# Kernel optimization log

Hardware: AMD Instinct MI355X
Metric: run time of the kernel (lower is better)

## Reference

```python
import jax, jax.numpy as jnp
import numpy as np
import math

B, N, L, ED, H = 2, 32, 4, 64, 4   # graphs, nodes/graph, layers, embed_dim, heads
HD = ED // H
EPS = 1e-5


def _ln(x, g, b):
    m = x.mean(-1, keepdims=True)
    v = ((x - m) ** 2).mean(-1, keepdims=True)
    return (x - m) * jax.lax.rsqrt(v + EPS) * g + b


def _layer(x, W, b, lg, lb, fW, fb, fg, fbeta):
    # NOTE: in the torch source, ModuleList([Linear]*4) shares ONE linear for
    # q/k/v1/v2 and ONE LayerNorm for norms[0..2]; we reproduce that sharing.
    h = (x @ W.T + b).reshape(B, N, N, H, HD)
    q = _ln(h, lg, lb)                                    # q == k (shared LN)
    scores = jnp.einsum('bxahd,bayhd->bxayh', q, q) / math.sqrt(HD)
    att = jax.nn.softmax(scores, axis=2)                  # softmax over 'a'
    xu = jnp.einsum('bxahd,bayhd->bxayhd', h, h)          # v1 == v2 == h
    xu = _ln(xu, lg, lb)                                  # shared LN again
    xu = jnp.einsum('bxayh,bxayhd->bxyhd', att, xu).reshape(B, N, N, ED)
    y = jnp.concatenate([x, xu], axis=-1) @ fW.T + fb
    return _ln(y, fg, fbeta)


def _diag_offdiag_maxpool(x):
    # x: (B, ED, N, N)
    diag = jnp.diagonal(x, axis1=-2, axis2=-1)            # (B, ED, N)
    max_diag = diag.max(axis=2)                           # (B, ED)
    val = jnp.abs(max_diag.max() + (-x).max())
    eye = jnp.eye(N, dtype=x.dtype)
    max_offdiag = (x - val * eye).max(axis=(2, 3))        # (B, ED)
    return jnp.concatenate([max_diag, max_offdiag], axis=1)  # (B, 2*ED)


def setup_inputs() -> dict:
    key = jax.random.key(0)
    ks = jax.random.split(key, 12)
    E = 1024
    g = jax.random.randint(ks[0], (E,), 0, B)
    ls = jax.random.randint(ks[1], (E,), 0, N)
    ld = jax.random.randint(ks[2], (E,), 0, N)
    edge_index = jnp.stack([g * N + ls, g * N + ld]).astype(jnp.int64)
    batch = (jnp.arange(B * N) // N).astype(jnp.int64)
    std = 0.02
    return {
        'edge_index': edge_index,
        'batch': batch,
        'W0': jax.random.normal(ks[3], (ED, 1), jnp.float32) * std,
        'b0': jnp.zeros((ED,), jnp.float32),
        'Ws': jax.random.normal(ks[4], (L - 1, ED, ED), jnp.float32) * std,
        'bs': jnp.zeros((L - 1, ED), jnp.float32),
        'ln_g': jnp.ones((L, HD), jnp.float32),
        'ln_b': jnp.zeros((L, HD), jnp.float32),
        'fW0': jax.random.normal(ks[5], (ED, 1 + ED), jnp.float32) * std,
        'fb0': jnp.zeros((ED,), jnp.float32),
        'fWs': jax.random.normal(ks[6], (L - 1, ED, 2 * ED), jnp.float32) * std,
        'fbs': jnp.zeros((L - 1, ED), jnp.float32),
        'fln_g': jnp.ones((L, ED), jnp.float32),
        'fln_b': jnp.zeros((L, ED), jnp.float32),
        'opW': jax.random.normal(ks[7], (L, ED // 2, 2 * ED), jnp.float32) * std,
        'opb': jnp.zeros((L, ED // 2), jnp.float32),
    }


def reference(edge_index, batch, W0, b0, Ws, bs, ln_g, ln_b,
              fW0, fb0, fWs, fbs, fln_g, fln_b, opW, opb):
    # to_dense_adj with edge_attr = 1.0
    g = batch[edge_index[0]]
    ls = edge_index[0] - g * N
    ld = edge_index[1] - g * N
    adj = jnp.zeros((B, N, N), jnp.float32).at[g, ls, ld].add(1.0)
    idx = jnp.arange(N)
    adj = adj.at[:, idx, idx].set(2.0)
    x = adj[..., None]                                    # (B, N, N, 1)

    scores = jnp.zeros((B, ED // 2), jnp.float32)
    for i in range(L):
        W = W0 if i == 0 else Ws[i - 1]
        b = b0 if i == 0 else bs[i - 1]
        fW = fW0 if i == 0 else fWs[i - 1]
        fb = fb0 if i == 0 else fbs[i - 1]
        x = _layer(x, W, b, ln_g[i], ln_b[i], fW, fb, fln_g[i], fln_b[i])
        pooled = _diag_offdiag_maxpool(jnp.transpose(x, (0, 3, 1, 2)))
        scores = scores + pooled @ opW[i].T + opb[i]

    # BatchNorm1d(momentum=1.0, affine=False), training mode -> batch stats
    m = scores.mean(axis=0)
    v = scores.var(axis=0)
    return (scores - m) / jnp.sqrt(v + EPS)
```

## Files before the change

kernel.cpp:

```cpp
#include <hip/hip_runtime.h>
#include <math.h>

#define EPS 1e-5f

#define AG_LOAD(p)     __hip_atomic_load((p), __ATOMIC_RELAXED, __HIP_MEMORY_SCOPE_AGENT)

__device__ __forceinline__ unsigned fenc(float f) {
    unsigned u = __float_as_uint(f);
    return (u & 0x80000000u) ? ~u : (u | 0x80000000u);
}
__device__ __forceinline__ float fdec(unsigned u) {
    u = (u & 0x80000000u) ? (u & 0x7FFFFFFFu) : ~u;
    return __uint_as_float(u);
}

struct Params {
    const int* ei; const int* batch; int E;
    const float* W0; const float* b0; const float* Ws; const float* bs;
    const float* ln_g; const float* ln_b;
    const float* fW0; const float* fb0; const float* fWs; const float* fbs;
    const float* fln_g; const float* fln_b;
    const float* opW; const float* opb;
    float* hA; float* hAT;
    float* hB; float* hBT;
    float* xbuf;
    unsigned* PdgU; unsigned* PoffU; unsigned* PmnU;
    int* bar;
    float* out;
};


__device__ __forceinline__ void pool_atomic(Params& p, int layer, int b_blk, int e,
                                            float mn, float off, float dg) {
    int o = layer * 128 + b_blk * 64 + e;
    atomicMax(&p.PdgU[o],  fenc(dg));
    atomicMax(&p.PoffU[o], fenc(off));
    atomicMax(&p.PmnU[o],  fenc(-mn));
}

__launch_bounds__(256, 2)
__global__ void k0(Params p) {
    const int tid  = threadIdx.x;
    const int blk  = blockIdx.x;
    const int gtid = blk * 256 + tid;
    const int c    = tid & 63;
    const int d    = c & 15;
    const int rl   = tid >> 6;
    const int rx   = rl >> 1;
    const int ry   = rl & 1;
    const int b_blk = blk >> 8;
    const int x0    = ((blk >> 4) & 15) * 2;
    const int y0    = (blk & 15) * 2;
    const int a_l  = c & 31;
    const int h1   = c >> 5;

    __shared__ float xslab2[2 * 32];
    __shared__ float yslab2[32 * 2];
    __shared__ __align__(16) float cA[64], cC[64], cW[64], cB0[64], cG[64], cBl[64];
    __shared__ float hstat[3][4];
    __shared__ float A1_s[4 * 132];
    __shared__ float K0h_s[4][4];
    __shared__ __align__(16) float xrow[4][64];
    __shared__ __align__(16) float xu_s[4][64];
    __shared__ float Wf0[64];
    __shared__ __align__(16) float T65[64 * 68];
    __shared__ __align__(16) float ST[64 * 68];

    if (tid < 64)  xslab2[tid] = 0.0f;
    if (tid >= 64 && tid < 128) yslab2[tid - 64] = 0.0f;

    if (tid < 64) {
        float Wc = p.W0[c], bc = p.b0[c];
        float sW = Wc, sB = bc;
        #pragma unroll
        for (int m = 1; m < 16; m <<= 1) {
            sW += __shfl_xor(sW, m, 16);
            sB += __shfl_xor(sB, m, 16);
        }
        float Ac = Wc - sW * 0.0625f;
        float Bc = bc - sB * 0.0625f;
        float sAA = Ac * Ac, sAB = Ac * Bc, sBB = Bc * Bc;
        #pragma unroll
        for (int m = 1; m < 16; m <<= 1) {
            sAA += __shfl_xor(sAA, m, 16);
            sAB += __shfl_xor(sAB, m, 16);
            sBB += __shfl_xor(sBB, m, 16);
        }
        cA[c] = Ac; cC[c] = Bc; cW[c] = Wc; cB0[c] = bc;
        cG[c] = p.ln_g[d]; cBl[c] = p.ln_b[d];
        if (d == 0) {
            hstat[0][c >> 4] = sAA * 0.0625f;
            hstat[1][c >> 4] = sAB * 0.0625f;
            hstat[2][c >> 4] = sBB * 0.0625f;
        }
        Wf0[tid] = p.fW0[tid * 65];
    }
    #pragma unroll
    for (int s = 0; s < 4; ++s) {
        int i = tid + s * 256;
        int cc = i >> 4, u = i & 15;
        const float* src = p.fW0 + cc * 65 + 1 + 4 * u;
        float4 w = make_float4(src[0], src[1], src[2], src[3]);
        *(float4*)(T65 + cc * 68 + 4 * ((u + 2 * cc) & 15)) = w;
    }
    #pragma unroll
    for (int s = 0; s < 4; ++s) {
        int i = tid + s * 256;
        float4 w = ((const float4*)p.Ws)[i];
        int cc = i >> 4, u = i & 15;
        *(float4*)(ST + cc * 68 + 4 * ((u + 2 * cc) & 15)) = w;
    }
    __syncthreads();

    for (int e2 = tid; e2 < p.E; e2 += 256) {
        int e0 = p.ei[e2], e1 = p.ei[p.E + e2];
        int g  = p.batch[e0];
        if (g == b_blk) {
            int ls = e0 - g * 32, ld = e1 - g * 32;
            unsigned dx = (unsigned)(ls - x0);
            if (dx < 2u) atomicAdd(&xslab2[dx * 32 + ld], 1.0f);
            unsigned dy = (unsigned)(ld - y0);
            if (dy < 2u) atomicAdd(&yslab2[ls * 2 + dy], 1.0f);
        }
    }
    __syncthreads();
    if (tid < 2)  xslab2[tid * 32 + x0 + tid] = 2.0f;
    if (tid >= 2 && tid < 4) { int j = tid - 2; yslab2[(y0 + j) * 2 + j] = 2.0f; }
    __syncthreads();

    const float vx = xslab2[rx * 32 + a_l];
    const float vy = yslab2[a_l * 2 + ry];
    float s0, s1, is0, is1, w0m, w1m;
    #pragma unroll
    for (int hb = 0; hb < 2; ++hb) {
        const int hh = h1 + 2 * hb;
        float rsx = rsqrtf(fmaf(fmaf(hstat[0][hh], vx, 2.0f * hstat[1][hh]), vx, hstat[2][hh]) + EPS);
        float rsy = rsqrtf(fmaf(fmaf(hstat[0][hh], vy, 2.0f * hstat[1][hh]), vy, hstat[2][hh]) + EPS);
        float qq = 0.f, sp = 0.f, sq = 0.f;
        #pragma unroll
        for (int t = 0; t < 4; ++t) {
            int dd = hh * 16 + 4 * t;
            float4 av = *(const float4*)(cA + dd);
            float4 bv = *(const float4*)(cC + dd);
            float4 wv = *(const float4*)(cW + dd);
            float4 b0v = *(const float4*)(cB0 + dd);
            float4 gv = *(const float4*)(cG + dd);
            float4 blv = *(const float4*)(cBl + dd);
            float qx, qy, pp;
            qx = fmaf(av.x, vx, bv.x) * rsx * gv.x + blv.x;
            qy = fmaf(av.x, vy, bv.x) * rsy * gv.x + blv.x;
            qq = fmaf(qx, qy, qq);
            pp = fmaf(wv.x, vx, b0v.x) * fmaf(wv.x, vy, b0v.x); sp += pp; sq += pp * pp;
            qx = fmaf(av.y, vx, bv.y) * rsx * gv.y + blv.y;
            qy = fmaf(av.y, vy, bv.y) * rsy * gv.y + blv.y;
            qq = fmaf(qx, qy, qq);
            pp = fmaf(wv.y, vx, b0v.y) * fmaf(wv.y, vy, b0v.y); sp += pp; sq += pp * pp;
            qx = fmaf(av.z, vx, bv.z) * rsx * gv.z + blv.z;
            qy = fmaf(av.z, vy, bv.z) * rsy * gv.z + blv.z;
            qq = fmaf(qx, qy, qq);
            pp = fmaf(wv.z, vx, b0v.z) * fmaf(wv.z, vy, b0v.z); sp += pp; sq += pp * pp;
            qx = fmaf(av.w, vx, bv.w) * rsx * gv.w + blv.w;
            qy = fmaf(av.w, vy, bv.w) * rsy * gv.w + blv.w;
            qq = fmaf(qx, qy, qq);
            pp = fmaf(wv.w, vx, b0v.w) * fmaf(wv.w, vy, b0v.w); sp += pp; sq += pp * pp;
        }
        float ss = qq * 0.25f;
        float mu = sp * 0.0625f, var = fmaxf(sq * 0.0625f - mu * mu, 0.f);
        float is = rsqrtf(var + EPS);
        if (hb == 0) { s0 = ss; is0 = is; w0m = mu * is; }
        else         { s1 = ss; is1 = is; w1m = mu * is; }
    }

    float m0 = s0, m1 = s1;
    #pragma unroll
    for (int m = 1; m < 32; m <<= 1) {
        m0 = fmaxf(m0, __shfl_xor(m0, m));
        m1 = fmaxf(m1, __shfl_xor(m1, m));
    }
    float e0 = __expf(s0 - m0), e1 = __expf(s1 - m1);
    float l0 = e0, l1 = e1, k0a = e0 * w0m, k1a = e1 * w1m;
    #pragma unroll
    for (int m = 1; m < 32; m <<= 1) {
        l0 += __shfl_xor(l0, m);  l1 += __shfl_xor(l1, m);
        k0a += __shfl_xor(k0a, m); k1a += __shfl_xor(k1a, m);
    }
    A1_s[rl * 132 + h1 * 33 + a_l]       = e0 * is0 / l0;
    A1_s[rl * 132 + (h1 + 2) * 33 + a_l] = e1 * is1 / l1;
    if (a_l == 0) {
        K0h_s[rl][h1]     = k0a / l0;
        K0h_s[rl][h1 + 2] = k1a / l1;
    }

    {
        const int hc = c >> 4;
        const float Wc = cW[c], bc = cB0[c];
        float acc = 0.f;
        #pragma unroll
        for (int a = 0; a < 32; ++a) {
            float vx2 = xslab2[rx * 32 + a];
            float vy2 = yslab2[a * 2 + ry];
            float pv = fmaf(Wc, vx2, bc) * fmaf(Wc, vy2, bc);
            acc = fmaf(A1_s[rl * 132 + hc * 33 + a], pv, acc);
        }
        xu_s[rl][c] = (acc - K0h_s[rl][hc]) * cG[c] + cBl[c];
    }

    const float adjv = xslab2[rx * 32 + y0 + ry];
    float acc2 = fmaf(Wf0[c], adjv, p.fb0[c]);
    #pragma unroll
    for (int u = 0; u < 16; ++u) {
        float4 w = *(const float4*)(T65 + c * 68 + 4 * ((u + 2 * c) & 15));
        float4 xr = *(const float4*)(&xu_s[rl][4 * u]);
        acc2 = fmaf(w.x, xr.x, acc2); acc2 = fmaf(w.y, xr.y, acc2);
        acc2 = fmaf(w.z, xr.z, acc2); acc2 = fmaf(w.w, xr.w, acc2);
    }
    float t1 = acc2;
    #pragma unroll
    for (int m = 1; m < 64; m <<= 1) t1 += __shfl_xor(t1, m, 64);
    float mu = t1 * (1.0f / 64.0f);
    float dv2 = acc2 - mu;
    float t2 = dv2 * dv2;
    #pragma unroll
    for (int m = 1; m < 64; m <<= 1) t2 += __shfl_xor(t2, m, 64);
    float xnew = dv2 * rsqrtf(t2 * (1.0f / 64.0f) + EPS) * p.fln_g[c] + p.fln_b[c];
    xrow[rl][c]  = xnew;
    p.xbuf[gtid] = xnew;
    __syncthreads();

    if (tid < 64) {
        float mn = 1e30f, off = -1e30f, dg = -1e30f;
        #pragma unroll
        for (int r2 = 0; r2 < 4; ++r2) {
            float v = xrow[r2][tid];
            mn = fminf(mn, v);
            if (x0 + (r2 >> 1) == y0 + (r2 & 1)) dg = fmaxf(dg, v);
            else off = fmaxf(off, v);
        }
        pool_atomic(p, 0, b_blk, tid, mn, off, dg);
    }

    {
        float acc = p.bs[c];
        #pragma unroll
        for (int u = 0; u < 16; ++u) {
            float4 w = *(const float4*)(ST + c * 68 + 4 * ((u + 2 * c) & 15));
            float4 xr = *(const float4*)(&xrow[rl][4 * u]);
            acc = fmaf(w.x, xr.x, acc); acc = fmaf(w.y, xr.y, acc);
            acc = fmaf(w.z, xr.z, acc); acc = fmaf(w.w, xr.w, acc);
        }
        int x = x0 + rx, y = y0 + ry;
        p.hA[(b_blk * 1024 + x * 32 + y) * 64 + c] = acc;
        p.hAT[((b_blk * 32 + y) * 32 + x) * 64 + c] = acc;
    }
}

__launch_bounds__(256, 2)
__global__ void klayer(Params p, int layer, int is_last) {
    const int tid  = threadIdx.x;
    const int blk  = blockIdx.x;
    const int gtid = blk * 256 + tid;
    const int c    = tid & 63;
    const int d    = c & 15;
    const int rl   = tid >> 6;
    const int rx   = rl >> 1;
    const int ry   = rl & 1;
    const int b_blk = blk >> 8;
    const int x0    = ((blk >> 4) & 15) * 2;
    const int y0    = (blk & 15) * 2;
    const int a_l  = c & 31;
    const int h1   = c >> 5;

    const float* hin  = (layer == 2) ? p.hB  : p.hA;
    const float* hinT = (layer == 2) ? p.hBT : p.hAT;
    float* hout  = (layer == 1) ? p.hB  : p.hA;
    float* houtT = (layer == 1) ? p.hBT : p.hAT;

    __shared__ __align__(16) float hx2_s[2][2176];
    __shared__ __align__(16) float yT2_s[2][2176];
    __shared__ __align__(16) float FT[64 * 132];
    __shared__ float A1_s[4 * 132];
    __shared__ float K0h_s[4][4];
    __shared__ __align__(16) float xrow[4][64];
    __shared__ __align__(16) float xu_s[4][64];
    __shared__ __align__(16) float g16[16], b16[16];
    __shared__ float vals[4];
    __shared__ float scores_s[64];
    __shared__ int tailflag;
    float* sm_mn  = &hx2_s[0][0];
    float* sm_off = sm_mn + 512;
    float* sm_dg  = sm_mn + 1024;
    float* psum   = sm_mn + 1536;

    float xv = p.xbuf[gtid];
    {
        const float4* sx0 = (const float4*)(hin + (b_blk * 1024 + x0 * 32) * 64);
        const float4* sx1 = (const float4*)(hin + (b_blk * 1024 + (x0 + 1) * 32) * 64);
        const float4* sy0 = (const float4*)(hinT + (b_blk * 32 + y0) * 2048);
        const float4* sy1 = (const float4*)(hinT + (b_blk * 32 + y0 + 1) * 2048);
        #pragma unroll
        for (int s = 0; s < 2; ++s) {
            int ii = tid + s * 256;
            int a = ii >> 4, u = ii & 15, pr = (u + 2 * a) & 15;
            *(float4*)(&hx2_s[0][a * 68 + 4 * pr]) = sx0[ii];
            *(float4*)(&hx2_s[1][a * 68 + 4 * pr]) = sx1[ii];
            *(float4*)(&yT2_s[0][a * 68 + 4 * pr]) = sy0[ii];
            *(float4*)(&yT2_s[1][a * 68 + 4 * pr]) = sy1[ii];
        }
    }
    if (tid < 16) {
        g16[tid] = p.ln_g[layer * 16 + tid];
        b16[tid] = p.ln_b[layer * 16 + tid];
    }
    {
        const float4* fw = (const float4*)(p.fWs + (layer - 1) * 8192);
        #pragma unroll
        for (int s = 0; s < 8; ++s) {
            int i = tid + s * 256;
            float4 w = fw[i];
            int cc = i >> 5, u = i & 31;
            *(float4*)(FT + cc * 132 + 4 * ((u + 2 * cc) & 31)) = w;
        }
    }
    xrow[rl][c] = xv;
    __syncthreads();

    float s0, s1, is0, is1, w0m, w1m;
    #pragma unroll
    for (int hb = 0; hb < 2; ++hb) {
        const int hh = h1 + 2 * hb;
        float4 xh4[4], yh4[4];
        float sxp = 0.f, sxq = 0.f, syp = 0.f, syq = 0.f;
        #pragma unroll
        for (int t = 0; t < 4; ++t) {
            int ps = 4 * (((hh * 4 + t) + 2 * a_l) & 15);
            float4 v = *(const float4*)(&hx2_s[rx][a_l * 68 + ps]);
            float4 y = *(const float4*)(&yT2_s[ry][a_l * 68 + ps]);
            xh4[t] = v; yh4[t] = y;
            sxp += v.x + v.y + v.z + v.w;
            sxq += v.x*v.x + v.y*v.y + v.z*v.z + v.w*v.w;
            syp += y.x + y.y + y.z + y.w;
            syq += y.x*y.x + y.y*y.y + y.z*y.z + y.w*y.w;
        }
        float mxm = sxp * 0.0625f;
        float rsx = rsqrtf(fmaxf(sxq * 0.0625f - mxm * mxm, 0.f) + EPS);
        float mym = syp * 0.0625f;
        float rsy = rsqrtf(fmaxf(syq * 0.0625f - mym * mym, 0.f) + EPS);
        float qq = 0.f, sp = 0.f, sq = 0.f;
        #pragma unroll
        for (int t = 0; t < 4; ++t) {
            float4 g4 = *(const float4*)(g16 + 4 * t);
            float4 b4 = *(const float4*)(b16 + 4 * t);
            float4 xh = xh4[t], yh = yh4[t];
            float qx, qy, pp;
            qx = (xh.x - mxm) * rsx * g4.x + b4.x;
            qy = (yh.x - mym) * rsy * g4.x + b4.x;
            qq = fmaf(qx, qy, qq);  pp = xh.x * yh.x; sp += pp; sq += pp * pp;
            qx = (xh.y - mxm) * rsx * g4.y + b4.y;
            qy = (yh.y - mym) * rsy * g4.y + b4.y;
            qq = fmaf(qx, qy, qq);  pp = xh.y * yh.y; sp += pp; sq += pp * pp;
            qx = (xh.z - mxm) * rsx * g4.z + b4.z;
            qy = (yh.z - mym) * rsy * g4.z + b4.z;
            qq = fmaf(qx, qy, qq);  pp = xh.z * yh.z; sp += pp; sq += pp * pp;
            qx = (xh.w - mxm) * rsx * g4.w + b4.w;
            qy = (yh.w - mym) * rsy * g4.w + b4.w;
            qq = fmaf(qx, qy, qq);  pp = xh.w * yh.w; sp += pp; sq += pp * pp;
        }
        float ss = qq * 0.25f;
        float mu = sp * 0.0625f, var = fmaxf(sq * 0.0625f - mu * mu, 0.f);
        float is = rsqrtf(var + EPS);
        if (hb == 0) { s0 = ss; is0 = is; w0m = mu * is; }
        else         { s1 = ss; is1 = is; w1m = mu * is; }
    }

    float m0 = s0, m1 = s1;
    #pragma unroll
    for (int m = 1; m < 32; m <<= 1) {
        m0 = fmaxf(m0, __shfl_xor(m0, m));
        m1 = fmaxf(m1, __shfl_xor(m1, m));
    }
    float e0 = __expf(s0 - m0), e1 = __expf(s1 - m1);
    float l0 = e0, l1 = e1, k0a = e0 * w0m, k1a = e1 * w1m;
    #pragma unroll
    for (int m = 1; m < 32; m <<= 1) {
        l0 += __shfl_xor(l0, m);  l1 += __shfl_xor(l1, m);
        k0a += __shfl_xor(k0a, m); k1a += __shfl_xor(k1a, m);
    }
    A1_s[rl * 132 + h1 * 33 + a_l]       = e0 * is0 / l0;
    A1_s[rl * 132 + (h1 + 2) * 33 + a_l] = e1 * is1 / l1;
    if (a_l == 0) {
        K0h_s[rl][h1]     = k0a / l0;
        K0h_s[rl][h1 + 2] = k1a / l1;
    }

    {
        const int hc = c >> 4;
        const int ce = c & 3;
        float acc = 0.f;
        #pragma unroll
        for (int a = 0; a < 32; ++a) {
            int ps = 4 * (((c >> 2) + 2 * a) & 15) + ce;
            float hxv = hx2_s[rx][a * 68 + ps];
            float hyv = yT2_s[ry][a * 68 + ps];
            acc = fmaf(A1_s[rl * 132 + hc * 33 + a], hxv * hyv, acc);
        }
        xu_s[rl][c] = (acc - K0h_s[rl][hc]) * g16[d] + b16[d];
    }

    float acc2 = p.fbs[(layer - 1) * 64 + c];
    #pragma unroll
    for (int u = 0; u < 16; ++u) {
        float4 w = *(const float4*)(FT + c * 132 + 4 * ((u + 2 * c) & 31));
        float4 xr = *(const float4*)(&xrow[rl][4 * u]);
        acc2 = fmaf(w.x, xr.x, acc2); acc2 = fmaf(w.y, xr.y, acc2);
        acc2 = fmaf(w.z, xr.z, acc2); acc2 = fmaf(w.w, xr.w, acc2);
    }
    #pragma unroll
    for (int u = 16; u < 32; ++u) {
        float4 w = *(const float4*)(FT + c * 132 + 4 * ((u + 2 * c) & 31));
        float4 xr = *(const float4*)(&xu_s[rl][4 * (u - 16)]);
        acc2 = fmaf(w.x, xr.x, acc2); acc2 = fmaf(w.y, xr.y, acc2);
        acc2 = fmaf(w.z, xr.z, acc2); acc2 = fmaf(w.w, xr.w, acc2);
    }
    float t1 = acc2;
    #pragma unroll
    for (int m = 1; m < 64; m <<= 1) t1 += __shfl_xor(t1, m, 64);
    float mu = t1 * (1.0f / 64.0f);
    float dv2 = acc2 - mu;
    float t2 = dv2 * dv2;
    #pragma unroll
    for (int m = 1; m < 64; m <<= 1) t2 += __shfl_xor(t2, m, 64);
    float xnew = dv2 * rsqrtf(t2 * (1.0f / 64.0f) + EPS) *
                 p.fln_g[layer * 64 + c] + p.fln_b[layer * 64 + c];
    __syncthreads();
    xrow[rl][c] = xnew;
    if (!is_last) {
        p.xbuf[gtid] = xnew;
        const float4* sw = (const float4*)(p.Ws + layer * 4096);
        #pragma unroll
        for (int s = 0; s < 4; ++s) {
            int i = tid + s * 256;
            float4 w = sw[i];
            int cc = i >> 4, u = i & 15;
            *(float4*)(FT + cc * 68 + 4 * ((u + 2 * cc) & 15)) = w;
        }
    }
    __syncthreads();

    if (tid < 64) {
        float mn = 1e30f, off = -1e30f, dg = -1e30f;
        #pragma unroll
        for (int r2 = 0; r2 < 4; ++r2) {
            float v = xrow[r2][tid];
            mn = fminf(mn, v);
            if (x0 + (r2 >> 1) == y0 + (r2 & 1)) dg = fmaxf(dg, v);
            else off = fmaxf(off, v);
        }
        pool_atomic(p, layer, b_blk, tid, mn, off, dg);
    }

    if (!is_last) {
        float acc = p.bs[layer * 64 + c];
        #pragma unroll
        for (int u = 0; u < 16; ++u) {
            float4 w = *(const float4*)(FT + c * 68 + 4 * ((u + 2 * c) & 15));
            float4 xr = *(const float4*)(&xrow[rl][4 * u]);
            acc = fmaf(w.x, xr.x, acc); acc = fmaf(w.y, xr.y, acc);
            acc = fmaf(w.z, xr.z, acc); acc = fmaf(w.w, xr.w, acc);
        }
        int x = x0 + rx, y = y0 + ry;
        hout[(b_blk * 1024 + x * 32 + y) * 64 + c] = acc;
        houtT[((b_blk * 32 + y) * 32 + x) * 64 + c] = acc;
        return;
    }

    __syncthreads();
    if (tid == 0) {
        int r = __hip_atomic_fetch_add(p.bar, 1, __ATOMIC_RELAXED,
                                       __HIP_MEMORY_SCOPE_AGENT);
        tailflag = (r == 511) ? 1 : 0;
    }
    __syncthreads();
    if (!tailflag) return;

    #pragma unroll
    for (int s = 0; s < 2; ++s) {
        int slot = tid + s * 256;
        unsigned ud = AG_LOAD(&p.PdgU[slot]);
        unsigned uo = AG_LOAD(&p.PoffU[slot]);
        unsigned um = AG_LOAD(&p.PmnU[slot]);
        sm_dg[slot]  = fdec(ud);
        sm_off[slot] = fdec(uo);
        sm_mn[slot]  = -fdec(um);
    }
    __syncthreads();
    if (tid < 4) {
        float gmx = -1e30f, gmn = 1e30f;
        for (int i2 = 0; i2 < 128; ++i2) {
            gmx = fmaxf(gmx, sm_dg[tid * 128 + i2]);
            gmn = fminf(gmn, sm_mn[tid * 128 + i2]);
        }
        vals[tid] = fabsf(gmx - gmn);
    }
    __syncthreads();
    {
        int bb = tid >> 7, cc = (tid >> 2) & 31, pp = tid & 3;
        float a2 = 0.0f;
        for (int l = 0; l < 4; ++l) {
            float val = vals[l];
            const float* Wr = p.opW + l * 4096 + cc * 128;
            int base = l * 128 + bb * 64;
            for (int j = pp * 32; j < pp * 32 + 32; ++j) {
                float pv;
                if (j < 64) pv = sm_dg[base + j];
                else        pv = fmaxf(sm_off[base + j - 64], sm_dg[base + j - 64] - val);
                a2 = fmaf(Wr[j], pv, a2);
            }
        }
        psum[tid] = a2;
    }
    __syncthreads();
    if (tid < 64) {
        int bb = tid >> 5, cc = tid & 31;
        float a2 = 0.0f;
        for (int l = 0; l < 4; ++l) a2 += p.opb[l * 32 + cc];
        for (int pp = 0; pp < 4; ++pp) a2 += psum[bb * 128 + cc * 4 + pp];
        scores_s[tid] = a2;
    }
    __syncthreads();
    if (tid < 32) {
        float sA = scores_s[tid], sB = scores_s[32 + tid];
        float mu2 = 0.5f * (sA + sB);
        float va = 0.5f * ((sA - mu2) * (sA - mu2) + (sB - mu2) * (sB - mu2));
        float inv = rsqrtf(va + EPS);
        p.out[tid]      = (sA - mu2) * inv;
        p.out[32 + tid] = (sB - mu2) * inv;
    }
}

extern "C" void kernel_launch(void* const* d_in, const int* in_sizes, int n_in,
                              void* d_out, int out_size, void* d_ws, size_t ws_size,
                              hipStream_t stream) {
    Params prm;
    prm.ei    = (const int*)d_in[0];
    prm.batch = (const int*)d_in[1];
    prm.E     = in_sizes[0] / 2;
    prm.W0    = (const float*)d_in[2];
    prm.b0    = (const float*)d_in[3];
    prm.Ws    = (const float*)d_in[4];
    prm.bs    = (const float*)d_in[5];
    prm.ln_g  = (const float*)d_in[6];
    prm.ln_b  = (const float*)d_in[7];
    prm.fW0   = (const float*)d_in[8];
    prm.fb0   = (const float*)d_in[9];
    prm.fWs   = (const float*)d_in[10];
    prm.fbs   = (const float*)d_in[11];
    prm.fln_g = (const float*)d_in[12];
    prm.fln_b = (const float*)d_in[13];
    prm.opW   = (const float*)d_in[14];
    prm.opb   = (const float*)d_in[15];

    float* ws = (float*)d_ws;
    prm.hA    = ws;
    prm.hAT   = prm.hA   + 131072;
    prm.hB    = prm.hAT  + 131072;
    prm.hBT   = prm.hB   + 131072;
    prm.xbuf  = prm.hBT  + 131072;
    unsigned* pu = (unsigned*)(prm.xbuf + 131072);
    prm.PdgU  = pu;
    prm.PoffU = pu + 512;
    prm.PmnU  = pu + 1024;
    prm.bar   = (int*)(pu + 1536);
    prm.out   = (float*)d_out;

    hipMemsetAsync(pu, 0, 1552 * sizeof(unsigned), stream);
    k0<<<512, 256, 0, stream>>>(prm);
    klayer<<<512, 256, 0, stream>>>(prm, 1, 0);
    klayer<<<512, 256, 0, stream>>>(prm, 2, 0);
    klayer<<<512, 256, 0, stream>>>(prm, 3, 1);
}
```

Before: 160.7 us.

## Fuse layers 0 and 1 by recomputing layer-0 halo rows per block

Merges the first-layer kernel into the second layer. Each block rebuilds the full adjacency in shared memory and recomputes the layer-0 output for the 64 row and 64 column neighbours of its 2x2 tile (32 iterations per wave). It keeps the resulting layer-1 projections in shared slabs, so layer 1 runs without a launch boundary or a global round-trip. This removes one kernel launch and the hA/hAT traffic but adds heavy redundant compute and much larger shared memory, which may lower occupancy.

```diff
diff --git a/kernel.cpp b/kernel.cpp
--- a/kernel.cpp
+++ b/kernel.cpp
@@ -39,7 +39,7 @@
 }
 
 __launch_bounds__(256, 2)
-__global__ void k0(Params p) {
+__global__ void k1(Params p) {
     const int tid  = threadIdx.x;
     const int blk  = blockIdx.x;
     const int gtid = blk * 256 + tid;
@@ -54,21 +54,20 @@
     const int a_l  = c & 31;
     const int h1   = c >> 5;
 
-    __shared__ float xslab2[2 * 32];
-    __shared__ float yslab2[32 * 2];
+    __shared__ float adjm[32 * 33];
+    __shared__ __align__(16) float slabX[2][2176];
+    __shared__ __align__(16) float slabY[2][2176];
+    __shared__ __align__(16) float WB[8704];
     __shared__ __align__(16) float cA[64], cC[64], cW[64], cB0[64], cG[64], cBl[64];
     __shared__ float hstat[3][4];
+    __shared__ float Wf0[64];
     __shared__ float A1_s[4 * 132];
     __shared__ float K0h_s[4][4];
     __shared__ __align__(16) float xrow[4][64];
     __shared__ __align__(16) float xu_s[4][64];
-    __shared__ float Wf0[64];
-    __shared__ __align__(16) float T65[64 * 68];
-    __shared__ __align__(16) float ST[64 * 68];
-
-    if (tid < 64)  xslab2[tid] = 0.0f;
-    if (tid >= 64 && tid < 128) yslab2[tid - 64] = 0.0f;
-
+    __shared__ __align__(16) float g16[16], b16[16];
+
+    for (int i = tid; i < 1056; i += 256) adjm[i] = 0.0f;
     if (tid < 64) {
         float Wc = p.W0[c], bc = p.b0[c];
         float sW = Wc, sB = bc;
@@ -95,20 +94,24 @@
         }
         Wf0[tid] = p.fW0[tid * 65];
     }
+    if (tid < 16) {
+        g16[tid] = p.ln_g[16 + tid];
+        b16[tid] = p.ln_b[16 + tid];
+    }
     #pragma unroll
     for (int s = 0; s < 4; ++s) {
         int i = tid + s * 256;
         int cc = i >> 4, u = i & 15;
         const float* src = p.fW0 + cc * 65 + 1 + 4 * u;
         float4 w = make_float4(src[0], src[1], src[2], src[3]);
-        *(float4*)(T65 + cc * 68 + 4 * ((u + 2 * cc) & 15)) = w;
+        *(float4*)(WB + cc * 68 + 4 * ((u + 2 * cc) & 15)) = w;
     }
     #pragma unroll
     for (int s = 0; s < 4; ++s) {
         int i = tid + s * 256;
         float4 w = ((const float4*)p.Ws)[i];
         int cc = i >> 4, u = i & 15;
-        *(float4*)(ST + cc * 68 + 4 * ((u + 2 * cc) & 15)) = w;
+        *(float4*)(WB + 4352 + cc * 68 + 4 * ((u + 2 * cc) & 15)) = w;
     }
     __syncthreads();
 
@@ -117,52 +120,197 @@
         int g  = p.batch[e0];
         if (g == b_blk) {
             int ls = e0 - g * 32, ld = e1 - g * 32;
-            unsigned dx = (unsigned)(ls - x0);
-            if (dx < 2u) atomicAdd(&xslab2[dx * 32 + ld], 1.0f);
-            unsigned dy = (unsigned)(ld - y0);
-            if (dy < 2u) atomicAdd(&yslab2[ls * 2 + dy], 1.0f);
-        }
-    }
-    __syncthreads();
-    if (tid < 2)  xslab2[tid * 32 + x0 + tid] = 2.0f;
-    if (tid >= 2 && tid < 4) { int j = tid - 2; yslab2[(y0 + j) * 2 + j] = 2.0f; }
-    __syncthreads();
-
-    const float vx = xslab2[rx * 32 + a_l];
-    const float vy = yslab2[a_l * 2 + ry];
+            atomicAdd(&adjm[ls * 33 + ld], 1.0f);
+        }
+    }
+    __syncthreads();
+    if (tid < 32) adjm[tid * 33 + tid] = 2.0f;
+    __syncthreads();
+
+    #pragma unroll 1
+    for (int k = 0; k < 32; ++k) {
+        const int r = rl * 32 + k;
+        const bool isX = (r < 64);
+        const int rowx = isX ? (x0 + (r >> 5)) : ((r - 64) >> 1);
+        const int coly = isX ? (r & 31) : (y0 + ((r - 64) & 1));
+        const float vx = adjm[rowx * 33 + a_l];
+        const float vy = adjm[a_l * 33 + coly];
+
+        float s0, s1, is0, is1, w0m, w1m;
+        #pragma unroll
+        for (int hb = 0; hb < 2; ++hb) {
+            const int hh = h1 + 2 * hb;
+            float rsx = rsqrtf(fmaf(fmaf(hstat[0][hh], vx, 2.0f * hstat[1][hh]), vx, hstat[2][hh]) + EPS);
+            float rsy = rsqrtf(fmaf(fmaf(hstat[0][hh], vy, 2.0f * hstat[1][hh]), vy, hstat[2][hh]) + EPS);
+            float qq = 0.f, sp = 0.f, sq = 0.f;
+            #pragma unroll
+            for (int t = 0; t < 4; ++t) {
+                int dd = hh * 16 + 4 * t;
+                float4 av = *(const float4*)(cA + dd);
+                float4 bv = *(const float4*)(cC + dd);
+                float4 wv = *(const float4*)(cW + dd);
+                float4 b0v = *(const float4*)(cB0 + dd);
+                float4 gv = *(const float4*)(cG + dd);
+                float4 blv = *(const float4*)(cBl + dd);
+                float qx, qy, pp;
+                qx = fmaf(av.x, vx, bv.x) * rsx * gv.x + blv.x;
+                qy = fmaf(av.x, vy, bv.x) * rsy * gv.x + blv.x;
+                qq = fmaf(qx, qy, qq);
+                pp = fmaf(wv.x, vx, b0v.x) * fmaf(wv.x, vy, b0v.x); sp += pp; sq += pp * pp;
+                qx = fmaf(av.y, vx, bv.y) * rsx * gv.y + blv.y;
+                qy = fmaf(av.y, vy, bv.y) * rsy * gv.y + blv.y;
+                qq = fmaf(qx, qy, qq);
+                pp = fmaf(wv.y, vx, b0v.y) * fmaf(wv.y, vy, b0v.y); sp += pp; sq += pp * pp;
+                qx = fmaf(av.z, vx, bv.z) * rsx * gv.z + blv.z;
+                qy = fmaf(av.z, vy, bv.z) * rsy * gv.z + blv.z;
+                qq = fmaf(qx, qy, qq);
+                pp = fmaf(wv.z, vx, b0v.z) * fmaf(wv.z, vy, b0v.z); sp += pp; sq += pp * pp;
+                qx = fmaf(av.w, vx, bv.w) * rsx * gv.w + blv.w;
+                qy = fmaf(av.w, vy, bv.w) * rsy * gv.w + blv.w;
+                qq = fmaf(qx, qy, qq);
+                pp = fmaf(wv.w, vx, b0v.w) * fmaf(wv.w, vy, b0v.w); sp += pp; sq += pp * pp;
+            }
+            float ss = qq * 0.25f;
+            float mu = sp * 0.0625f, var = fmaxf(sq * 0.0625f - mu * mu, 0.f);
+            float is = rsqrtf(var + EPS);
+            if (hb == 0) { s0 = ss; is0 = is; w0m = mu * is; }
+            else         { s1 = ss; is1 = is; w1m = mu * is; }
+        }
+
+        float m0 = s0, m1 = s1;
+        #pragma unroll
+        for (int m = 1; m < 32; m <<= 1) {
+            m0 = fmaxf(m0, __shfl_xor(m0, m));
+            m1 = fmaxf(m1, __shfl_xor(m1, m));
+        }
+        float e0 = __expf(s0 - m0), e1 = __expf(s1 - m1);
+        float l0 = e0, l1 = e1, k0a = e0 * w0m, k1a = e1 * w1m;
+        #pragma unroll
+        for (int m = 1; m < 32; m <<= 1) {
+            l0 += __shfl_xor(l0, m);  l1 += __shfl_xor(l1, m);
+            k0a += __shfl_xor(k0a, m); k1a += __shfl_xor(k1a, m);
+        }
+        A1_s[rl * 132 + h1 * 33 + a_l]       = e0 * is0 / l0;
+        A1_s[rl * 132 + (h1 + 2) * 33 + a_l] = e1 * is1 / l1;
+        if (a_l == 0) {
+            K0h_s[rl][h1]     = k0a / l0;
+            K0h_s[rl][h1 + 2] = k1a / l1;
+        }
+
+        {
+            const int hc = c >> 4;
+            const float Wc = cW[c], bc = cB0[c];
+            float accp = 0.f;
+            #pragma unroll
+            for (int a = 0; a < 32; ++a) {
+                float vx2 = adjm[rowx * 33 + a];
+                float vy2 = adjm[a * 33 + coly];
+                float pv = fmaf(Wc, vx2, bc) * fmaf(Wc, vy2, bc);
+                accp = fmaf(A1_s[rl * 132 + hc * 33 + a], pv, accp);
+            }
+            xu_s[rl][c] = (accp - K0h_s[rl][hc]) * cG[c] + cBl[c];
+        }
+
+        const float adjv = adjm[rowx * 33 + coly];
+        float acc2 = fmaf(Wf0[c], adjv, p.fb0[c]);
+        #pragma unroll
+        for (int u = 0; u < 16; ++u) {
+            float4 w = *(const float4*)(WB + c * 68 + 4 * ((u + 2 * c) & 15));
+            float4 xr = *(const float4*)(&xu_s[rl][4 * u]);
+            acc2 = fmaf(w.x, xr.x, acc2); acc2 = fmaf(w.y, xr.y, acc2);
+            acc2 = fmaf(w.z, xr.z, acc2); acc2 = fmaf(w.w, xr.w, acc2);
+        }
+        float t1 = acc2;
+        #pragma unroll
+        for (int m = 1; m < 64; m <<= 1) t1 += __shfl_xor(t1, m, 64);
+        float mu = t1 * (1.0f / 64.0f);
+        float dv2 = acc2 - mu;
+        float t2 = dv2 * dv2;
+        #pragma unroll
+        for (int m = 1; m < 64; m <<= 1) t2 += __shfl_xor(t2, m, 64);
+        float x1c = dv2 * rsqrtf(t2 * (1.0f / 64.0f) + EPS) * p.fln_g[c] + p.fln_b[c];
+
+        if (isX && (unsigned)(coly - y0) < 2u)
+            xrow[(rowx - x0) * 2 + (coly - y0)][c] = x1c;
+        xu_s[rl][c] = x1c;
+
+        float acch = p.bs[c];
+        #pragma unroll
+        for (int u = 0; u < 16; ++u) {
+            float4 w = *(const float4*)(WB + 4352 + c * 68 + 4 * ((u + 2 * c) & 15));
+            float4 xr = *(const float4*)(&xu_s[rl][4 * u]);
+            acch = fmaf(w.x, xr.x, acch); acch = fmaf(w.y, xr.y, acch);
+            acch = fmaf(w.z, xr.z, acch); acch = fmaf(w.w, xr.w, acch);
+        }
+        float* srow = isX ? &slabX[r >> 5][0] : &slabY[(r - 64) & 1][0];
+        const int arow = isX ? (r & 31) : ((r - 64) >> 1);
+        srow[arow * 68 + 4 * (((c >> 2) + 2 * arow) & 15) + (c & 3)] = acch;
+    }
+    __syncthreads();
+
+    if (tid < 64) {
+        float mn = 1e30f, off = -1e30f, dg = -1e30f;
+        #pragma unroll
+        for (int r2 = 0; r2 < 4; ++r2) {
+            float v = xrow[r2][tid];
+            mn = fminf(mn, v);
+            if (x0 + (r2 >> 1) == y0 + (r2 & 1)) dg = fmaxf(dg, v);
+            else off = fmaxf(off, v);
+        }
+        pool_atomic(p, 0, b_blk, tid, mn, off, dg);
+    }
+    {
+        const float4* fw = (const float4*)(p.fWs);
+        #pragma unroll
+        for (int s = 0; s < 8; ++s) {
+            int i = tid + s * 256;
+            float4 w = fw[i];
+            int cc = i >> 5, u = i & 31;
+            *(float4*)(WB + cc * 132 + 4 * ((u + 2 * cc) & 31)) = w;
+        }
+    }
+    __syncthreads();
+
     float s0, s1, is0, is1, w0m, w1m;
     #pragma unroll
     for (int hb = 0; hb < 2; ++hb) {
         const int hh = h1 + 2 * hb;
-        float rsx = rsqrtf(fmaf(fmaf(hstat[0][hh], vx, 2.0f * hstat[1][hh]), vx, hstat[2][hh]) + EPS);
-        float rsy = rsqrtf(fmaf(fmaf(hstat[0][hh], vy, 2.0f * hstat[1][hh]), vy, hstat[2][hh]) + EPS);
+        float4 xh4[4], yh4[4];
+        float sxp = 0.f, sxq = 0.f, syp = 0.f, syq = 0.f;
+        #pragma unroll
+        for (int t = 0; t < 4; ++t) {
+            int ps = 4 * (((hh * 4 + t) + 2 * a_l) & 15);
+            float4 v = *(const float4*)(&slabX[rx][a_l * 68 + ps]);
+            float4 y = *(const float4*)(&slabY[ry][a_l * 68 + ps]);
+            xh4[t] = v; yh4[t] = y;
+            sxp += v.x + v.y + v.z + v.w;
+            sxq += v.x*v.x + v.y*v.y + v.z*v.z + v.w*v.w;
+            syp += y.x + y.y + y.z + y.w;
+            syq += y.x*y.x + y.y*y.y + y.z*y.z + y.w*y.w;
+        }
+        float mxm = sxp * 0.0625f;
+        float rsx = rsqrtf(fmaxf(sxq * 0.0625f - mxm * mxm, 0.f) + EPS);
+        float mym = syp * 0.0625f;
+        float rsy = rsqrtf(fmaxf(syq * 0.0625f - mym * mym, 0.f) + EPS);
         float qq = 0.f, sp = 0.f, sq = 0.f;
         #pragma unroll
         for (int t = 0; t < 4; ++t) {
-            int dd = hh * 16 + 4 * t;
-            float4 av = *(const float4*)(cA + dd);
-            float4 bv = *(const float4*)(cC + dd);
-            float4 wv = *(const float4*)(cW + dd);
-            float4 b0v = *(const float4*)(cB0 + dd);
-            float4 gv = *(const float4*)(cG + dd);
-            float4 blv = *(const float4*)(cBl + dd);
+            float4 g4 = *(const float4*)(g16 + 4 * t);
+            float4 b4 = *(const float4*)(b16 + 4 * t);
+            float4 xh = xh4[t], yh = yh4[t];
             float qx, qy, pp;
-            qx = fmaf(av.x, vx, bv.x) * rsx * gv.x + blv.x;
-            qy = fmaf(av.x, vy, bv.x) * rsy * gv.x + blv.x;
-            qq = fmaf(qx, qy, qq);
-            pp = fmaf(wv.x, vx, b0v.x) * fmaf(wv.x, vy, b0v.x); sp += pp; sq += pp * pp;
-            qx = fmaf(av.y, vx, bv.y) * rsx * gv.y + blv.y;
-            qy = fmaf(av.y, vy, bv.y) * rsy * gv.y + blv.y;
-            qq = fmaf(qx, qy, qq);
-            pp = fmaf(wv.y, vx, b0v.y) * fmaf(wv.y, vy, b0v.y); sp += pp; sq += pp * pp;
-            qx = fmaf(av.z, vx, bv.z) * rsx * gv.z + blv.z;
-            qy = fmaf(av.z, vy, bv.z) * rsy * gv.z + blv.z;
-            qq = fmaf(qx, qy, qq);
-            pp = fmaf(wv.z, vx, b0v.z) * fmaf(wv.z, vy, b0v.z); sp += pp; sq += pp * pp;
-            qx = fmaf(av.w, vx, bv.w) * rsx * gv.w + blv.w;
-            qy = fmaf(av.w, vy, bv.w) * rsy * gv.w + blv.w;
-            qq = fmaf(qx, qy, qq);
-            pp = fmaf(wv.w, vx, b0v.w) * fmaf(wv.w, vy, b0v.w); sp += pp; sq += pp * pp;
+            qx = (xh.x - mxm) * rsx * g4.x + b4.x;
+            qy = (yh.x - mym) * rsy * g4.x + b4.x;
+            qq = fmaf(qx, qy, qq);  pp = xh.x * yh.x; sp += pp; sq += pp * pp;
+            qx = (xh.y - mxm) * rsx * g4.y + b4.y;
+            qy = (yh.y - mym) * rsy * g4.y + b4.y;
+            qq = fmaf(qx, qy, qq);  pp = xh.y * yh.y; sp += pp; sq += pp * pp;
+            qx = (xh.z - mxm) * rsx * g4.z + b4.z;
+            qy = (yh.z - mym) * rsy * g4.z + b4.z;
+            qq = fmaf(qx, qy, qq);  pp = xh.z * yh.z; sp += pp; sq += pp * pp;
+            qx = (xh.w - mxm) * rsx * g4.w + b4.w;
+            qy = (yh.w - mym) * rsy * g4.w + b4.w;
+            qq = fmaf(qx, qy, qq);  pp = xh.w * yh.w; sp += pp; sq += pp * pp;
         }
         float ss = qq * 0.25f;
         float mu = sp * 0.0625f, var = fmaxf(sq * 0.0625f - mu * mu, 0.f);
@@ -170,7 +318,6 @@
         if (hb == 0) { s0 = ss; is0 = is; w0m = mu * is; }
         else         { s1 = ss; is1 = is; w1m = mu * is; }
     }
-
     float m0 = s0, m1 = s1;
     #pragma unroll
     for (int m = 1; m < 32; m <<= 1) {
@@ -190,27 +337,31 @@
         K0h_s[rl][h1]     = k0a / l0;
         K0h_s[rl][h1 + 2] = k1a / l1;
     }
-
     {
         const int hc = c >> 4;
-        const float Wc = cW[c], bc = cB0[c];
+        const int ce = c & 3;
         float acc = 0.f;
         #pragma unroll
         for (int a = 0; a < 32; ++a) {
-            float vx2 = xslab2[rx * 32 + a];
-            float vy2 = yslab2[a * 2 + ry];
-            float pv = fmaf(Wc, vx2, bc) * fmaf(Wc, vy2, bc);
-            acc = fmaf(A1_s[rl * 132 + hc * 33 + a], pv, acc);
-        }
-        xu_s[rl][c] = (acc - K0h_s[rl][hc]) * cG[c] + cBl[c];
-    }
-
-    const float adjv = xslab2[rx * 32 + y0 + ry];
-    float acc2 = fmaf(Wf0[c], adjv, p.fb0[c]);
+            int ps = 4 * (((c >> 2) + 2 * a) & 15) + ce;
+            float hxv = slabX[rx][a * 68 + ps];
+            float hyv = slabY[ry][a * 68 + ps];
+            acc = fmaf(A1_s[rl * 132 + hc * 33 + a], hxv * hyv, acc);
+        }
+        xu_s[rl][c] = (acc - K0h_s[rl][hc]) * g16[d] + b16[d];
+    }
+    float acc2 = p.fbs[c];
     #pragma unroll
     for (int u = 0; u < 16; ++u) {
-        float4 w = *(const float4*)(T65 + c * 68 + 4 * ((u + 2 * c) & 15));
-        float4 xr = *(const float4*)(&xu_s[rl][4 * u]);
+        float4 w = *(const float4*)(WB + c * 132 + 4 * ((u + 2 * c) & 31));
+        float4 xr = *(const float4*)(&xrow[rl][4 * u]);
+        acc2 = fmaf(w.x, xr.x, acc2); acc2 = fmaf(w.y, xr.y, acc2);
+        acc2 = fmaf(w.z, xr.z, acc2); acc2 = fmaf(w.w, xr.w, acc2);
+    }
+    #pragma unroll
+    for (int u = 16; u < 32; ++u) {
+        float4 w = *(const float4*)(WB + c * 132 + 4 * ((u + 2 * c) & 31));
+        float4 xr = *(const float4*)(&xu_s[rl][4 * (u - 16)]);
         acc2 = fmaf(w.x, xr.x, acc2); acc2 = fmaf(w.y, xr.y, acc2);
         acc2 = fmaf(w.z, xr.z, acc2); acc2 = fmaf(w.w, xr.w, acc2);
     }
@@ -222,9 +373,21 @@
     float t2 = dv2 * dv2;
     #pragma unroll
     for (int m = 1; m < 64; m <<= 1) t2 += __shfl_xor(t2, m, 64);
-    float xnew = dv2 * rsqrtf(t2 * (1.0f / 64.0f) + EPS) * p.fln_g[c] + p.fln_b[c];
-    xrow[rl][c]  = xnew;
+    float xnew = dv2 * rsqrtf(t2 * (1.0f / 64.0f) + EPS) *
+                 p.fln_g[64 + c] + p.fln_b[64 + c];
+    __syncthreads();
+    xrow[rl][c] = xnew;
     p.xbuf[gtid] = xnew;
+    {
+        const float4* sw = (const float4*)(p.Ws + 4096);
+        #pragma unroll
+        for (int s = 0; s < 4; ++s) {
+            int i = tid + s * 256;
+            float4 w = sw[i];
+            int cc = i >> 4, u = i & 15;
+            *(float4*)(WB + cc * 68 + 4 * ((u + 2 * cc) & 15)) = w;
+        }
+    }
     __syncthreads();
 
     if (tid < 64) {
@@ -236,21 +399,20 @@
             if (x0 + (r2 >> 1) == y0 + (r2 & 1)) dg = fmaxf(dg, v);
             else off = fmaxf(off, v);
         }
-        pool_atomic(p, 0, b_blk, tid, mn, off, dg);
-    }
-
+        pool_atomic(p, 1, b_blk, tid, mn, off, dg);
+    }
     {
-        float acc = p.bs[c];
+        float acc = p.bs[64 + c];
         #pragma unroll
         for (int u = 0; u < 16; ++u) {
-            float4 w = *(const float4*)(ST + c * 68 + 4 * ((u + 2 * c) & 15));
+            float4 w = *(const float4*)(WB + c * 68 + 4 * ((u + 2 * c) & 15));
             float4 xr = *(const float4*)(&xrow[rl][4 * u]);
             acc = fmaf(w.x, xr.x, acc); acc = fmaf(w.y, xr.y, acc);
             acc = fmaf(w.z, xr.z, acc); acc = fmaf(w.w, xr.w, acc);
         }
         int x = x0 + rx, y = y0 + ry;
-        p.hA[(b_blk * 1024 + x * 32 + y) * 64 + c] = acc;
-        p.hAT[((b_blk * 32 + y) * 32 + x) * 64 + c] = acc;
+        p.hB[(b_blk * 1024 + x * 32 + y) * 64 + c] = acc;
+        p.hBT[((b_blk * 32 + y) * 32 + x) * 64 + c] = acc;
     }
 }
 
@@ -573,8 +735,7 @@
     prm.out   = (float*)d_out;
 
     hipMemsetAsync(pu, 0, 1552 * sizeof(unsigned), stream);
-    k0<<<512, 256, 0, stream>>>(prm);
-    klayer<<<512, 256, 0, stream>>>(prm, 1, 0);
+    k1<<<512, 256, 0, stream>>>(prm);
     klayer<<<512, 256, 0, stream>>>(prm, 2, 0);
     klayer<<<512, 256, 0, stream>>>(prm, 3, 1);
 }
```

Result: slower. 559.9 us (+248.4%).
